# Optimization experiments

Measured on AMD Instinct MI355X. Metric: run time of the kernel, lower is better.

Reference implementation:

```python
import jax, jax.numpy as jnp
import numpy as np

D, H1, H2, OUT = 1024, 4096, 4096, 1


def _tanh_jet(a0, a1, a2):
    # 2nd-order Taylor-mode push-through of tanh:
    # u0 = tanh(a0); u1 = sech^2(a0)*a1; u2 = sech^2(a0)*a2 - 2*tanh(a0)*sech^2(a0)*a1^2
    u0 = jnp.tanh(a0)
    s = 1.0 - u0 * u0
    u1 = s * a1
    u2 = s * a2 - 2.0 * u0 * s * (a1 * a1)
    return u0, u1, u2


def setup_inputs() -> dict:
    key = jax.random.key(0)
    ks = jax.random.split(key, 7)
    x = jax.random.normal(ks[0], (D,), dtype=jnp.float32)
    # Kaiming-like scaling so tanh stays in its nonlinear regime
    W1 = jax.random.normal(ks[1], (H1, D), dtype=jnp.float32) / np.sqrt(D)
    b1 = jax.random.normal(ks[2], (H1,), dtype=jnp.float32) * 0.01
    W2 = jax.random.normal(ks[3], (H2, H1), dtype=jnp.float32) / np.sqrt(H1)
    b2 = jax.random.normal(ks[4], (H2,), dtype=jnp.float32) * 0.01
    W3 = jax.random.normal(ks[5], (OUT, H2), dtype=jnp.float32) / np.sqrt(H2)
    b3 = jax.random.normal(ks[6], (OUT,), dtype=jnp.float32) * 0.01
    return {"x": x, "W1": W1, "b1": b1, "W2": W2, "b2": b2, "W3": W3, "b3": b3}


def reference(x, W1, b1, W2, b2, W3, b3):
    # propagated simultaneously over all D basis tangent vectors (vectorized vmap).
    d = x.shape[0]
    X1 = jnp.eye(d, dtype=x.dtype)            # [D, D] basis tangents; x2 = 0
    # layer 1 (linear): primal broadcasts over the tangent batch
    a0 = x @ W1.T + b1                         # [H1]
    a1 = X1 @ W1.T                             # [D, H1]
    a2 = jnp.zeros_like(a1)                    # second input coefficient is zero
    u0, u1, u2 = _tanh_jet(a0, a1, a2)
    # layer 2 (linear)
    z0 = u0 @ W2.T + b2                        # [H2]
    z1 = u1 @ W2.T                             # [D, H2]
    z2 = u2 @ W2.T                             # [D, H2]
    v0, v1, v2 = _tanh_jet(z0, z1, z2)
    # layer 3 (linear); F2[i] = e_i^T H_f(x) e_i
    F2 = v2 @ W3.T                             # [D, 1]
    return F2.sum(0)                           # [1] = trace(H_f) = Laplacian
```

## Files before the change

### kernel.cpp

```cpp
#include <hip/hip_runtime.h>
#include <math.h>

#define DD 1024
#define HH1 4096
#define HH2 4096

typedef __attribute__((ext_vector_type(8))) short bf16x8;
typedef __attribute__((ext_vector_type(4))) float f32x4;
typedef unsigned short ushort_t;

#define WS_FAST_BYTES 42008576ull
#define K4_LDS_BYTES (131072 + 64)

__device__ inline void wave_reduce2(float& a, float& b) {
  #pragma unroll
  for (int off = 32; off > 0; off >>= 1) {
    a += __shfl_down(a, off, 64);
    b += __shfl_down(b, off, 64);
  }
}

__device__ inline unsigned int f2b(float f) {
  union { float f; unsigned int u; } v; v.f = f;
  return (v.u + 0x7FFFu + ((v.u >> 16) & 1u)) >> 16;
}
__device__ inline unsigned int pack2(float a, float b) {
  return f2b(a) | (f2b(b) << 16);
}

__device__ inline void gl_lds16(const void* g, void* l) {
  __builtin_amdgcn_global_load_lds(
      (const __attribute__((address_space(1))) unsigned int*)g,
      (__attribute__((address_space(3))) unsigned int*)l, 16, 0, 0);
}

__global__ __launch_bounds__(256) void kA2a_l1(
    const float* __restrict__ W1, const float* __restrict__ x,
    const float* __restrict__ b1, float* __restrict__ u0,
    float* __restrict__ q) {
  const int h = blockIdx.x;
  const int tid = threadIdx.x;
  const float4 w = ((const float4*)(W1 + (size_t)h * DD))[tid];
  const float4 xv = ((const float4*)x)[tid];
  float dot = w.x * xv.x + w.y * xv.y + w.z * xv.z + w.w * xv.w;
  float sq  = w.x * w.x + w.y * w.y + w.z * w.z + w.w * w.w;
  wave_reduce2(dot, sq);
  __shared__ float lds[8];
  const int lane = tid & 63, wid = tid >> 6;
  if (lane == 0) { lds[wid * 2] = dot; lds[wid * 2 + 1] = sq; }
  __syncthreads();
  if (tid == 0) {
    float dsum = lds[0] + lds[2] + lds[4] + lds[6];
    float rsum = lds[1] + lds[3] + lds[5] + lds[7];
    float a0 = dsum + b1[h];
    float u = tanhf(a0);
    float s = 1.f - u * u;
    u0[h] = u;
    q[h] = -2.f * u * s * rsum;
  }
}

#define TP 516
__global__ __launch_bounds__(256) void kA2b_t(
    const float* __restrict__ W1, ushort_t* __restrict__ Bp) {
  __shared__ ushort_t T[32 * TP];
  const int tid = threadIdx.x;
  const int h0 = (blockIdx.x >> 1) * 32;
  const int i0 = (blockIdx.x & 1) * 512;
  #pragma unroll
  for (int it = 0; it < 16; ++it) {
    const int lin = it * 256 + tid;
    const int r = lin >> 7;
    const int c4 = lin & 127;
    float4 w = *(const float4*)(W1 + (size_t)(h0 + r) * DD + i0 + c4 * 4);
    uint2 pk;
    pk.x = pack2(w.x, w.y);
    pk.y = pack2(w.z, w.w);
    *(uint2*)&T[r * TP + c4 * 4] = pk;
  }
  __syncthreads();
  const int ip = tid * 2;
  #pragma unroll
  for (int c = 0; c < 4; ++c) {
    unsigned int R[8];
    #pragma unroll
    for (int r8 = 0; r8 < 8; ++r8)
      R[r8] = *(const unsigned int*)&T[(c * 8 + r8) * TP + ip];
    unsigned int oa[4], ob[4];
    #pragma unroll
    for (int k2 = 0; k2 < 4; ++k2) {
      oa[k2] = (R[2 * k2] & 0xffffu) | (R[2 * k2 + 1] << 16);
      ob[k2] = (R[2 * k2] >> 16) | (R[2 * k2 + 1] & 0xffff0000u);
    }
    *(uint4*)(Bp + (size_t)(i0 + ip) * HH1 + h0 + c * 8) = *(const uint4*)oa;
    *(uint4*)(Bp + (size_t)(i0 + ip + 1) * HH1 + h0 + c * 8) = *(const uint4*)ob;
  }
}

__global__ __launch_bounds__(256) void k0a_layer2conv(
    const float* __restrict__ W2, const float* __restrict__ b2,
    const float* __restrict__ W3, const float* __restrict__ u0,
    const float* __restrict__ q, ushort_t* __restrict__ Ap,
    float* __restrict__ cv, float* __restrict__ cd) {
  int g = blockIdx.x;
  int tid = threadIdx.x;
  const float4* row = (const float4*)(W2 + (size_t)g * HH1);
  const float4* u4 = (const float4*)u0;
  const float4* q4 = (const float4*)q;
  float zacc = 0.f, dacc = 0.f;
  #pragma unroll
  for (int it = 0; it < 4; ++it) {
    int j = tid + it * 256;
    float4 w = row[j];
    float4 u = u4[j];
    float4 qq = q4[j];
    float4 sv;
    sv.x = 1.f - u.x * u.x;
    sv.y = 1.f - u.y * u.y;
    sv.z = 1.f - u.z * u.z;
    sv.w = 1.f - u.w * u.w;
    zacc += w.x * u.x + w.y * u.y + w.z * u.z + w.w * u.w;
    dacc += w.x * qq.x + w.y * qq.y + w.z * qq.z + w.w * qq.w;
    uint2 pk;
    pk.x = pack2(w.x * sv.x, w.y * sv.y);
    pk.y = pack2(w.z * sv.z, w.w * sv.w);
    *(uint2*)(Ap + (size_t)g * HH1 + j * 4) = pk;
  }
  wave_reduce2(zacc, dacc);
  __shared__ float lds[8];
  int lane = tid & 63, wid = tid >> 6;
  if (lane == 0) { lds[wid * 2] = zacc; lds[wid * 2 + 1] = dacc; }
  __syncthreads();
  if (tid == 0) {
    float z = lds[0] + lds[2] + lds[4] + lds[6] + b2[g];
    float d = lds[1] + lds[3] + lds[5] + lds[7];
    float v = tanhf(z);
    float t = 1.f - v * v;
    float c = W3[g] * t;
    cv[g] = c * v;
    cd[g] = c * d;
  }
}

__global__ __launch_bounds__(512) void k4_bt64q(
    const ushort_t* __restrict__ Ap, const ushort_t* __restrict__ Bp,
    const float* __restrict__ cv, float* __restrict__ P) {
  extern __shared__ __align__(16) char smem[];
  char* const Ab0 = smem;
  char* const Bb0 = smem + 65536;
  float* const red = (float*)(smem + 131072);

  const int tid = threadIdx.x;
  const int lane = tid & 63;
  const int wave = tid >> 6;
  const int wm = wave >> 1;
  const int wn = wave & 1;
  const int l = blockIdx.x;
  const int xcd = l & 7;
  const int jj = l >> 3;
  const int g0 = (xcd * 4 + (jj & 3)) * 128;
  const int i0 = (jj >> 2) * 128;

  const int srow = lane >> 3;
  const int schunk = (lane & 7) ^ srow;
  const size_t agbase = (size_t)(g0 + srow) * HH1 + schunk * 8;
  const size_t bgbase = (size_t)(i0 + srow) * HH1 + schunk * 8;

  const int fr = lane & 15;
  const int fc = lane >> 4;
  const int rsw = fr & 7;

  f32x4 acc[2][4];
  const f32x4 zero = {0.f, 0.f, 0.f, 0.f};
  #pragma unroll
  for (int mt = 0; mt < 2; ++mt)
    #pragma unroll
    for (int nt = 0; nt < 4; ++nt) acc[mt][nt] = zero;

  #define STAGE_PAIR(tile, sub) do {                                        \
      const int buf_ = (tile) & 3;                                          \
      const int r0_ = wave * 16 + (sub) * 8;                                \
      const size_t koff_ = (size_t)(((tile) & 63) * 64);                    \
      gl_lds16(Ap + agbase + (size_t)r0_ * HH1 + koff_,                     \
               Ab0 + buf_ * 16384 + r0_ * 128);                             \
      gl_lds16(Bp + bgbase + (size_t)r0_ * HH1 + koff_,                     \
               Bb0 + buf_ * 16384 + r0_ * 128);                             \
    } while (0)

  STAGE_PAIR(0, 0); STAGE_PAIR(0, 1);
  STAGE_PAIR(1, 0); STAGE_PAIR(1, 1);
  STAGE_PAIR(2, 0); STAGE_PAIR(2, 1);

  for (int t = 0; t < 64; ++t) {
    const int buf = t & 3;
    const char* Abuf = Ab0 + buf * 16384;
    const char* Bbuf = Bb0 + buf * 16384;
    asm volatile("s_waitcnt vmcnt(8)" ::: "memory");
    __builtin_amdgcn_s_barrier();
    asm volatile("" ::: "memory");
    #pragma unroll
    for (int kk = 0; kk < 2; ++kk) {
      STAGE_PAIR(t + 3, kk);
      bf16x8 af[2], bfv[4];
      #pragma unroll
      for (int mt = 0; mt < 2; ++mt) {
        const int row = wm * 32 + mt * 16 + fr;
        af[mt] = *(const bf16x8*)(Abuf + row * 128 + (((kk * 4 + fc) ^ rsw) * 16));
      }
      #pragma unroll
      for (int nt = 0; nt < 4; ++nt) {
        const int row = wn * 64 + nt * 16 + fr;
        bfv[nt] = *(const bf16x8*)(Bbuf + row * 128 + (((kk * 4 + fc) ^ rsw) * 16));
      }
      __builtin_amdgcn_s_setprio(1);
      #pragma unroll
      for (int mt = 0; mt < 2; ++mt)
        #pragma unroll
        for (int nt = 0; nt < 4; ++nt)
          acc[mt][nt] = __builtin_amdgcn_mfma_f32_16x16x32_bf16(
              af[mt], bfv[nt], acc[mt][nt], 0, 0, 0);
      __builtin_amdgcn_s_setprio(0);
      if (kk == 0) __builtin_amdgcn_s_barrier();
    }
  }
  #undef STAGE_PAIR

  float part = 0.f;
  #pragma unroll
  for (int mt = 0; mt < 2; ++mt) {
    #pragma unroll
    for (int r = 0; r < 4; ++r) {
      const int g = g0 + wm * 32 + mt * 16 + fc * 4 + r;
      const float c = cv[g];
      float ss = 0.f;
      #pragma unroll
      for (int nt = 0; nt < 4; ++nt) {
        float v = acc[mt][nt][r];
        ss += v * v;
      }
      part += c * ss;
    }
  }
  #pragma unroll
  for (int off = 32; off > 0; off >>= 1) part += __shfl_down(part, off, 64);
  if (lane == 0) red[wave] = part;
  __syncthreads();
  if (tid == 0) {
    float s = 0.f;
    #pragma unroll
    for (int w2 = 0; w2 < 8; ++w2) s += red[w2];
    P[l] = s;
  }
}

__global__ __launch_bounds__(256) void k5_final(
    const float* __restrict__ cd, const float* __restrict__ P,
    float* __restrict__ out) {
  int tid = threadIdx.x;
  float a = 0.f;
  for (int j = tid; j < HH2; j += 256) a += cd[j];
  float b = P[tid];
  float v = a - 2.f * b;
  #pragma unroll
  for (int off = 32; off > 0; off >>= 1) v += __shfl_down(v, off, 64);
  __shared__ float lds[4];
  int lane = tid & 63, wid = tid >> 6;
  if (lane == 0) lds[wid] = v;
  __syncthreads();
  if (tid == 0) out[0] = lds[0] + lds[1] + lds[2] + lds[3];
}


__global__ __launch_bounds__(256) void k1_slow(
    const float* __restrict__ W1, const float* __restrict__ x,
    const float* __restrict__ b1, float* __restrict__ u0,
    float* __restrict__ q, float* __restrict__ s_out,
    float* __restrict__ out) {
  int h = blockIdx.x;
  int tid = threadIdx.x;
  const float4* row = (const float4*)(W1 + (size_t)h * DD);
  const float4* x4 = (const float4*)x;
  float4 w = row[tid];
  float4 xv = x4[tid];
  float dot = w.x * xv.x + w.y * xv.y + w.z * xv.z + w.w * xv.w;
  float sq = w.x * w.x + w.y * w.y + w.z * w.z + w.w * w.w;
  wave_reduce2(dot, sq);
  __shared__ float lds[8];
  int lane = tid & 63, wid = tid >> 6;
  if (lane == 0) { lds[wid * 2] = dot; lds[wid * 2 + 1] = sq; }
  __syncthreads();
  if (tid == 0) {
    float dsum = lds[0] + lds[2] + lds[4] + lds[6];
    float rsum = lds[1] + lds[3] + lds[5] + lds[7];
    float a0 = dsum + b1[h];
    float u = tanhf(a0);
    float s = 1.f - u * u;
    u0[h] = u;
    s_out[h] = s;
    q[h] = -2.f * u * s * rsum;
    if (h == 0) out[0] = 0.f;
  }
}

__global__ __launch_bounds__(256) void k2_slow(
    const float* __restrict__ W2, const float* __restrict__ b2,
    const float* __restrict__ W3, const float* __restrict__ u0,
    const float* __restrict__ q, float* __restrict__ cv,
    float* __restrict__ out) {
  int g = blockIdx.x;
  int tid = threadIdx.x;
  const float4* row = (const float4*)(W2 + (size_t)g * HH1);
  const float4* u4 = (const float4*)u0;
  const float4* q4 = (const float4*)q;
  float zacc = 0.f, dacc = 0.f;
  for (int j = tid; j < HH1 / 4; j += 256) {
    float4 w = row[j];
    float4 u = u4[j];
    float4 qq = q4[j];
    zacc += w.x * u.x + w.y * u.y + w.z * u.z + w.w * u.w;
    dacc += w.x * qq.x + w.y * qq.y + w.z * qq.z + w.w * qq.w;
  }
  wave_reduce2(zacc, dacc);
  __shared__ float lds[8];
  int lane = tid & 63, wid = tid >> 6;
  if (lane == 0) { lds[wid * 2] = zacc; lds[wid * 2 + 1] = dacc; }
  __syncthreads();
  if (tid == 0) {
    float z = lds[0] + lds[2] + lds[4] + lds[6] + b2[g];
    float d = lds[1] + lds[3] + lds[5] + lds[7];
    float v = tanhf(z);
    float t = 1.f - v * v;
    float c = W3[g] * t;
    cv[g] = c * v;
    atomicAdd(out, c * d);
  }
}

__global__ __launch_bounds__(256) void k4_slow(
    const float* __restrict__ W2, const float* __restrict__ W1,
    const float* __restrict__ s, const float* __restrict__ cv,
    float* __restrict__ out) {
  __shared__ float As[32][68];
  __shared__ float Bs[32][68];
  int tid = threadIdx.x;
  int g0 = blockIdx.y * 64;
  int i0 = blockIdx.x * 64;
  int tr = (tid / 16) * 4;
  int tc = (tid % 16) * 4;
  float acc[4][4] = {};
  for (int k0 = 0; k0 < HH1; k0 += 32) {
    for (int ll = tid; ll < (64 * 32 / 4); ll += 256) {
      int row = ll / 8;
      int c4 = ll % 8;
      float4 w = *(const float4*)(W2 + (size_t)(g0 + row) * HH1 + k0 + c4 * 4);
      float4 sv = *(const float4*)(s + k0 + c4 * 4);
      As[c4 * 4 + 0][row] = w.x * sv.x;
      As[c4 * 4 + 1][row] = w.y * sv.y;
      As[c4 * 4 + 2][row] = w.z * sv.z;
      As[c4 * 4 + 3][row] = w.w * sv.w;
    }
    for (int ll = tid; ll < (32 * 64 / 4); ll += 256) {
      int row = ll / 16;
      int c4 = ll % 16;
      float4 w = *(const float4*)(W1 + (size_t)(k0 + row) * DD + i0 + c4 * 4);
      *(float4*)&Bs[row][c4 * 4] = w;
    }
    __syncthreads();
    #pragma unroll
    for (int k = 0; k < 32; ++k) {
      float4 av = *(const float4*)&As[k][tr];
      float4 bv = *(const float4*)&Bs[k][tc];
      float a_[4] = {av.x, av.y, av.z, av.w};
      float b_[4] = {bv.x, bv.y, bv.z, bv.w};
      #pragma unroll
      for (int r = 0; r < 4; ++r)
        #pragma unroll
        for (int c = 0; c < 4; ++c)
          acc[r][c] += a_[r] * b_[c];
    }
    __syncthreads();
  }
  float contrib = 0.f;
  #pragma unroll
  for (int r = 0; r < 4; ++r) {
    float ss = acc[r][0] * acc[r][0] + acc[r][1] * acc[r][1] +
               acc[r][2] * acc[r][2] + acc[r][3] * acc[r][3];
    contrib += cv[g0 + tr + r] * ss;
  }
  #pragma unroll
  for (int off = 32; off > 0; off >>= 1) contrib += __shfl_down(contrib, off, 64);
  __shared__ float red[4];
  int lane = tid & 63, wid = tid >> 6;
  if (lane == 0) red[wid] = contrib;
  __syncthreads();
  if (tid == 0) atomicAdd(out, -2.f * (red[0] + red[1] + red[2] + red[3]));
}

extern "C" void kernel_launch(void* const* d_in, const int* in_sizes, int n_in,
                              void* d_out, int out_size, void* d_ws, size_t ws_size,
                              hipStream_t stream) {
  const float* x  = (const float*)d_in[0];
  const float* W1 = (const float*)d_in[1];
  const float* b1 = (const float*)d_in[2];
  const float* W2 = (const float*)d_in[3];
  const float* b2 = (const float*)d_in[4];
  const float* W3 = (const float*)d_in[5];
  float* out = (float*)d_out;
  float* ws = (float*)d_ws;

  if (ws_size >= WS_FAST_BYTES) {
    float* u0 = ws;
    float* q  = ws + 4096;
    float* cv = ws + 8192;
    float* cd = ws + 12288;
    float* P  = ws;
    ushort_t* Ap = (ushort_t*)((char*)d_ws + 65536);
    ushort_t* Bp = (ushort_t*)((char*)d_ws + 33619968);
    hipFuncSetAttribute((const void*)k4_bt64q,
                        hipFuncAttributeMaxDynamicSharedMemorySize,
                        K4_LDS_BYTES);
    hipLaunchKernelGGL(kA2a_l1, dim3(HH1), dim3(256), 0, stream,
                       W1, x, b1, u0, q);
    hipLaunchKernelGGL(kA2b_t, dim3(256), dim3(256), 0, stream, W1, Bp);
    hipLaunchKernelGGL(k0a_layer2conv, dim3(HH2), dim3(256), 0, stream,
                       W2, b2, W3, u0, q, Ap, cv, cd);
    hipLaunchKernelGGL(k4_bt64q, dim3(256), dim3(512), K4_LDS_BYTES, stream,
                       Ap, Bp, cv, P);
    hipLaunchKernelGGL(k5_final, dim3(1), dim3(256), 0, stream, cd, P, out);
  } else {
    float* u0 = ws;
    float* q  = ws + 4096;
    float* s  = ws + 8192;
    float* cv = ws + 12288;
    hipLaunchKernelGGL(k1_slow, dim3(HH1), dim3(256), 0, stream,
                       W1, x, b1, u0, q, s, out);
    hipLaunchKernelGGL(k2_slow, dim3(HH2), dim3(256), 0, stream,
                       W2, b2, W3, u0, q, cv, out);
    hipLaunchKernelGGL(k4_slow, dim3(DD / 64, HH2 / 64), dim3(256), 0, stream,
                       W2, W1, s, cv, out);
  }
}
```

Baseline: 177.1 us.

## Use 32x32 MFMA with split-K wave groups and atomic final reduction

Rewrites the main GEMM kernel to use 32x32x16 bf16 MFMA tiles. The 8 waves are split into two groups that each handle alternate K tiles, with the two partial accumulators combined through LDS at the end. The final reduction kernel is dropped: the per-g correction term and the per-block partial sums are now added directly to the output with atomics, and the output is zeroed in the first kernel. This cuts LDS fragment loads per MFMA and removes one launch, at the cost of an extra LDS exchange and a float atomic ordering that is not deterministic.

```diff
diff --git a/kernel.cpp b/kernel.cpp
--- a/kernel.cpp
+++ b/kernel.cpp
@@ -7,10 +7,11 @@
 
 typedef __attribute__((ext_vector_type(8))) short bf16x8;
 typedef __attribute__((ext_vector_type(4))) float f32x4;
+typedef __attribute__((ext_vector_type(16))) float f32x16;
 typedef unsigned short ushort_t;
 
 #define WS_FAST_BYTES 42008576ull
-#define K4_LDS_BYTES (131072 + 64)
+#define K4_LDS_BYTES 131072
 
 __device__ inline void wave_reduce2(float& a, float& b) {
   #pragma unroll
@@ -37,9 +38,10 @@
 __global__ __launch_bounds__(256) void kA2a_l1(
     const float* __restrict__ W1, const float* __restrict__ x,
     const float* __restrict__ b1, float* __restrict__ u0,
-    float* __restrict__ q) {
+    float* __restrict__ q, float* __restrict__ out) {
   const int h = blockIdx.x;
   const int tid = threadIdx.x;
+  if (h == 0 && tid == 0) out[0] = 0.f;
   const float4 w = ((const float4*)(W1 + (size_t)h * DD))[tid];
   const float4 xv = ((const float4*)x)[tid];
   float dot = w.x * xv.x + w.y * xv.y + w.z * xv.z + w.w * xv.w;
@@ -101,7 +103,7 @@
     const float* __restrict__ W2, const float* __restrict__ b2,
     const float* __restrict__ W3, const float* __restrict__ u0,
     const float* __restrict__ q, ushort_t* __restrict__ Ap,
-    float* __restrict__ cv, float* __restrict__ cd) {
+    float* __restrict__ cv, float* __restrict__ out) {
   int g = blockIdx.x;
   int tid = threadIdx.x;
   const float4* row = (const float4*)(W2 + (size_t)g * HH1);
@@ -138,23 +140,21 @@
     float t = 1.f - v * v;
     float c = W3[g] * t;
     cv[g] = c * v;
-    cd[g] = c * d;
-  }
-}
-
-__global__ __launch_bounds__(512) void k4_bt64q(
+    atomicAdd(out, c * d);
+  }
+}
+
+__global__ __launch_bounds__(512) void k4_v3(
     const ushort_t* __restrict__ Ap, const ushort_t* __restrict__ Bp,
-    const float* __restrict__ cv, float* __restrict__ P) {
+    const float* __restrict__ cv, float* __restrict__ out) {
   extern __shared__ __align__(16) char smem[];
-  char* const Ab0 = smem;
-  char* const Bb0 = smem + 65536;
-  float* const red = (float*)(smem + 131072);
 
   const int tid = threadIdx.x;
   const int lane = tid & 63;
   const int wave = tid >> 6;
-  const int wm = wave >> 1;
-  const int wn = wave & 1;
+  const int gp = wave >> 2;
+  const int wq = wave & 3;
+  const int wm = wq >> 1, wn = wq & 1;
   const int l = blockIdx.x;
   const int xcd = l & 7;
   const int jj = l >> 3;
@@ -162,112 +162,112 @@
   const int i0 = (jj >> 2) * 128;
 
   const int srow = lane >> 3;
-  const int schunk = (lane & 7) ^ srow;
-  const size_t agbase = (size_t)(g0 + srow) * HH1 + schunk * 8;
-  const size_t bgbase = (size_t)(i0 + srow) * HH1 + schunk * 8;
-
-  const int fr = lane & 15;
-  const int fc = lane >> 4;
-  const int rsw = fr & 7;
-
-  f32x4 acc[2][4];
-  const f32x4 zero = {0.f, 0.f, 0.f, 0.f};
+  const int lchunk = (lane & 7) ^ srow;
+  const ushort_t* gA0 = Ap + (size_t)(g0 + wave * 16 + 0 + srow) * HH1 + lchunk * 8;
+  const ushort_t* gA1 = Ap + (size_t)(g0 + wave * 16 + 8 + srow) * HH1 + lchunk * 8;
+  const ushort_t* gB0 = Bp + (size_t)(i0 + wave * 16 + 0 + srow) * HH1 + lchunk * 8;
+  const ushort_t* gB1 = Bp + (size_t)(i0 + wave * 16 + 8 + srow) * HH1 + lchunk * 8;
+
+  const int half = lane >> 5;
+  const int r7 = lane & 7;
+  const int rowA0 = (wm * 64 + (lane & 31)) * 128;
+  const int rowA1 = rowA0 + 32 * 128;
+  const int rowB0 = 16384 + (wn * 64 + (lane & 31)) * 128;
+  const int rowB1 = rowB0 + 32 * 128;
+
+  f32x16 acc[2][2];
   #pragma unroll
   for (int mt = 0; mt < 2; ++mt)
     #pragma unroll
-    for (int nt = 0; nt < 4; ++nt) acc[mt][nt] = zero;
-
-  #define STAGE_PAIR(tile, sub) do {                                        \
-      const int buf_ = (tile) & 3;                                          \
-      const int r0_ = wave * 16 + (sub) * 8;                                \
-      const size_t koff_ = (size_t)(((tile) & 63) * 64);                    \
-      gl_lds16(Ap + agbase + (size_t)r0_ * HH1 + koff_,                     \
-               Ab0 + buf_ * 16384 + r0_ * 128);                             \
-      gl_lds16(Bp + bgbase + (size_t)r0_ * HH1 + koff_,                     \
-               Bb0 + buf_ * 16384 + r0_ * 128);                             \
+    for (int nt = 0; nt < 2; ++nt)
+      #pragma unroll
+      for (int r = 0; r < 16; ++r) acc[mt][nt][r] = 0.f;
+
+  #define STAGE(tile) do {                                              \
+      char* tb_ = smem + ((tile) & 3) * 32768;                          \
+      const int ko_ = ((tile) & 63) * 64;                               \
+      gl_lds16(gA0 + ko_, tb_ + (wave * 16 + 0) * 128 + lane * 16);     \
+      gl_lds16(gA1 + ko_, tb_ + (wave * 16 + 8) * 128 + lane * 16);     \
+      gl_lds16(gB0 + ko_, tb_ + 16384 + (wave * 16 + 0) * 128 + lane * 16); \
+      gl_lds16(gB1 + ko_, tb_ + 16384 + (wave * 16 + 8) * 128 + lane * 16); \
     } while (0)
 
-  STAGE_PAIR(0, 0); STAGE_PAIR(0, 1);
-  STAGE_PAIR(1, 0); STAGE_PAIR(1, 1);
-  STAGE_PAIR(2, 0); STAGE_PAIR(2, 1);
-
-  for (int t = 0; t < 64; ++t) {
-    const int buf = t & 3;
-    const char* Abuf = Ab0 + buf * 16384;
-    const char* Bbuf = Bb0 + buf * 16384;
+  STAGE(0); STAGE(1);
+  for (int s = 0; s < 32; ++s) {
+    STAGE(2 * s + 2);
+    STAGE(2 * s + 3);
     asm volatile("s_waitcnt vmcnt(8)" ::: "memory");
     __builtin_amdgcn_s_barrier();
     asm volatile("" ::: "memory");
-    #pragma unroll
-    for (int kk = 0; kk < 2; ++kk) {
-      STAGE_PAIR(t + 3, kk);
-      bf16x8 af[2], bfv[4];
+    const char* tb = smem + ((2 * s + gp) & 3) * 32768;
+    #pragma unroll
+    for (int kk = 0; kk < 4; ++kk) {
+      const int cb = ((kk * 2 + half) ^ r7) * 16;
+      bf16x8 af[2], bfv[2];
+      af[0]  = *(const bf16x8*)(tb + rowA0 + cb);
+      af[1]  = *(const bf16x8*)(tb + rowA1 + cb);
+      bfv[0] = *(const bf16x8*)(tb + rowB0 + cb);
+      bfv[1] = *(const bf16x8*)(tb + rowB1 + cb);
+      __builtin_amdgcn_s_setprio(1);
+      acc[0][0] = __builtin_amdgcn_mfma_f32_32x32x16_bf16(af[0], bfv[0], acc[0][0], 0, 0, 0);
+      acc[0][1] = __builtin_amdgcn_mfma_f32_32x32x16_bf16(af[0], bfv[1], acc[0][1], 0, 0, 0);
+      acc[1][0] = __builtin_amdgcn_mfma_f32_32x32x16_bf16(af[1], bfv[0], acc[1][0], 0, 0, 0);
+      acc[1][1] = __builtin_amdgcn_mfma_f32_32x32x16_bf16(af[1], bfv[1], acc[1][1], 0, 0, 0);
+      __builtin_amdgcn_s_setprio(0);
+    }
+    asm volatile("" ::: "memory");
+    __builtin_amdgcn_s_barrier();
+  }
+  #undef STAGE
+
+  asm volatile("s_waitcnt vmcnt(0)" ::: "memory");
+  __builtin_amdgcn_s_barrier();
+
+  char* xz = smem + 65536 + wq * 16384;
+  if (gp == 1) {
+    #pragma unroll
+    for (int qd = 0; qd < 16; ++qd) {
+      const int mt = qd >> 3, nt = (qd >> 2) & 1, r0 = (qd & 3) * 4;
+      float4 v;
+      v.x = acc[mt][nt][r0 + 0];
+      v.y = acc[mt][nt][r0 + 1];
+      v.z = acc[mt][nt][r0 + 2];
+      v.w = acc[mt][nt][r0 + 3];
+      *(float4*)(xz + qd * 1024 + ((lane + qd) & 63) * 16) = v;
+    }
+  }
+  __syncthreads();
+  if (gp == 0) {
+    #pragma unroll
+    for (int qd = 0; qd < 16; ++qd) {
+      const int mt = qd >> 3, nt = (qd >> 2) & 1, r0 = (qd & 3) * 4;
+      float4 v = *(const float4*)(xz + qd * 1024 + ((lane + qd) & 63) * 16);
+      acc[mt][nt][r0 + 0] += v.x;
+      acc[mt][nt][r0 + 1] += v.y;
+      acc[mt][nt][r0 + 2] += v.z;
+      acc[mt][nt][r0 + 3] += v.w;
+    }
+    float part = 0.f;
+    #pragma unroll
+    for (int mt = 0; mt < 2; ++mt) {
       #pragma unroll
-      for (int mt = 0; mt < 2; ++mt) {
-        const int row = wm * 32 + mt * 16 + fr;
-        af[mt] = *(const bf16x8*)(Abuf + row * 128 + (((kk * 4 + fc) ^ rsw) * 16));
+      for (int r = 0; r < 16; ++r) {
+        const int g = g0 + wm * 64 + mt * 32 + (r & 3) + 8 * (r >> 2) + 4 * half;
+        const float c = cv[g];
+        const float m0 = acc[mt][0][r];
+        const float m1 = acc[mt][1][r];
+        part += c * (m0 * m0 + m1 * m1);
       }
-      #pragma unroll
-      for (int nt = 0; nt < 4; ++nt) {
-        const int row = wn * 64 + nt * 16 + fr;
-        bfv[nt] = *(const bf16x8*)(Bbuf + row * 128 + (((kk * 4 + fc) ^ rsw) * 16));
-      }
-      __builtin_amdgcn_s_setprio(1);
-      #pragma unroll
-      for (int mt = 0; mt < 2; ++mt)
-        #pragma unroll
-        for (int nt = 0; nt < 4; ++nt)
-          acc[mt][nt] = __builtin_amdgcn_mfma_f32_16x16x32_bf16(
-              af[mt], bfv[nt], acc[mt][nt], 0, 0, 0);
-      __builtin_amdgcn_s_setprio(0);
-      if (kk == 0) __builtin_amdgcn_s_barrier();
-    }
-  }
-  #undef STAGE_PAIR
-
-  float part = 0.f;
-  #pragma unroll
-  for (int mt = 0; mt < 2; ++mt) {
-    #pragma unroll
-    for (int r = 0; r < 4; ++r) {
-      const int g = g0 + wm * 32 + mt * 16 + fc * 4 + r;
-      const float c = cv[g];
-      float ss = 0.f;
-      #pragma unroll
-      for (int nt = 0; nt < 4; ++nt) {
-        float v = acc[mt][nt][r];
-        ss += v * v;
-      }
-      part += c * ss;
-    }
-  }
-  #pragma unroll
-  for (int off = 32; off > 0; off >>= 1) part += __shfl_down(part, off, 64);
-  if (lane == 0) red[wave] = part;
+    }
+    #pragma unroll
+    for (int off = 32; off > 0; off >>= 1) part += __shfl_down(part, off, 64);
+    if (lane == 0) ((float*)smem)[wq] = part;
+  }
   __syncthreads();
   if (tid == 0) {
-    float s = 0.f;
-    #pragma unroll
-    for (int w2 = 0; w2 < 8; ++w2) s += red[w2];
-    P[l] = s;
-  }
-}
-
-__global__ __launch_bounds__(256) void k5_final(
-    const float* __restrict__ cd, const float* __restrict__ P,
-    float* __restrict__ out) {
-  int tid = threadIdx.x;
-  float a = 0.f;
-  for (int j = tid; j < HH2; j += 256) a += cd[j];
-  float b = P[tid];
-  float v = a - 2.f * b;
-  #pragma unroll
-  for (int off = 32; off > 0; off >>= 1) v += __shfl_down(v, off, 64);
-  __shared__ float lds[4];
-  int lane = tid & 63, wid = tid >> 6;
-  if (lane == 0) lds[wid] = v;
-  __syncthreads();
-  if (tid == 0) out[0] = lds[0] + lds[1] + lds[2] + lds[3];
+    float* rp = (float*)smem;
+    atomicAdd(out, -2.f * (rp[0] + rp[1] + rp[2] + rp[3]));
+  }
 }
 
 
@@ -412,21 +412,18 @@
     float* u0 = ws;
     float* q  = ws + 4096;
     float* cv = ws + 8192;
-    float* cd = ws + 12288;
-    float* P  = ws;
     ushort_t* Ap = (ushort_t*)((char*)d_ws + 65536);
     ushort_t* Bp = (ushort_t*)((char*)d_ws + 33619968);
-    hipFuncSetAttribute((const void*)k4_bt64q,
+    hipFuncSetAttribute((const void*)k4_v3,
                         hipFuncAttributeMaxDynamicSharedMemorySize,
                         K4_LDS_BYTES);
     hipLaunchKernelGGL(kA2a_l1, dim3(HH1), dim3(256), 0, stream,
-                       W1, x, b1, u0, q);
+                       W1, x, b1, u0, q, out);
     hipLaunchKernelGGL(kA2b_t, dim3(256), dim3(256), 0, stream, W1, Bp);
     hipLaunchKernelGGL(k0a_layer2conv, dim3(HH2), dim3(256), 0, stream,
-                       W2, b2, W3, u0, q, Ap, cv, cd);
-    hipLaunchKernelGGL(k4_bt64q, dim3(256), dim3(512), K4_LDS_BYTES, stream,
-                       Ap, Bp, cv, P);
-    hipLaunchKernelGGL(k5_final, dim3(1), dim3(256), 0, stream, cd, P, out);
+                       W2, b2, W3, u0, q, Ap, cv, out);
+    hipLaunchKernelGGL(k4_v3, dim3(256), dim3(512), K4_LDS_BYTES, stream,
+                       Ap, Bp, cv, out);
   } else {
     float* u0 = ws;
     float* q  = ws + 4096;
```

Result: slower. 208.8 us (+17.9%).

## Fuse layer-1 jet reduction with W1 bf16 transpose into one kernel

Applied to the files above, without the earlier changes.

Merges the layer-1 dot/sumsq kernel and the W1 bf16 transpose kernel into a single kernel, so W1 is read from global memory once instead of twice and one launch is removed. Each block now handles 16 rows over the full 1024 columns, with a 16-lane shuffle reduction. Separately, the layer-2 conversion kernel issues all of its W2/u0/q loads up front to raise memory-level parallelism. The trade-offs are fewer rows per block (256 blocks total) and more registers held in the layer-2 kernel.

```diff
diff --git a/kernel.cpp b/kernel.cpp
--- a/kernel.cpp
+++ b/kernel.cpp
@@ -34,66 +34,62 @@
       (__attribute__((address_space(3))) unsigned int*)l, 16, 0, 0);
 }
 
-__global__ __launch_bounds__(256) void kA2a_l1(
+#define TP2 1032
+__global__ __launch_bounds__(256) void kA3_l1t(
     const float* __restrict__ W1, const float* __restrict__ x,
     const float* __restrict__ b1, float* __restrict__ u0,
-    float* __restrict__ q) {
-  const int h = blockIdx.x;
+    float* __restrict__ q, ushort_t* __restrict__ Bp) {
+  __shared__ __align__(16) ushort_t T[16 * TP2];
   const int tid = threadIdx.x;
-  const float4 w = ((const float4*)(W1 + (size_t)h * DD))[tid];
-  const float4 xv = ((const float4*)x)[tid];
-  float dot = w.x * xv.x + w.y * xv.y + w.z * xv.z + w.w * xv.w;
-  float sq  = w.x * w.x + w.y * w.y + w.z * w.z + w.w * w.w;
-  wave_reduce2(dot, sq);
-  __shared__ float lds[8];
-  const int lane = tid & 63, wid = tid >> 6;
-  if (lane == 0) { lds[wid * 2] = dot; lds[wid * 2 + 1] = sq; }
-  __syncthreads();
-  if (tid == 0) {
-    float dsum = lds[0] + lds[2] + lds[4] + lds[6];
-    float rsum = lds[1] + lds[3] + lds[5] + lds[7];
-    float a0 = dsum + b1[h];
+  const int h0 = blockIdx.x * 16;
+  const int r = tid >> 4;
+  const int c = tid & 15;
+  const float4* rp = (const float4*)(W1 + (size_t)(h0 + r) * DD);
+  const float4* x4 = (const float4*)x;
+  float dot = 0.f, sq = 0.f;
+  #pragma unroll
+  for (int j = 0; j < 16; ++j) {
+    const int f = c + j * 16;
+    float4 wv = rp[f];
+    float4 xv = x4[f];
+    dot += wv.x * xv.x + wv.y * xv.y + wv.z * xv.z + wv.w * xv.w;
+    sq  += wv.x * wv.x + wv.y * wv.y + wv.z * wv.z + wv.w * wv.w;
+    uint2 pk;
+    pk.x = pack2(wv.x, wv.y);
+    pk.y = pack2(wv.z, wv.w);
+    *(uint2*)&T[r * TP2 + f * 4] = pk;
+  }
+  #pragma unroll
+  for (int off = 8; off > 0; off >>= 1) {
+    dot += __shfl_down(dot, off, 16);
+    sq  += __shfl_down(sq, off, 16);
+  }
+  if (c == 0) {
+    float a0 = dot + b1[h0 + r];
     float u = tanhf(a0);
     float s = 1.f - u * u;
-    u0[h] = u;
-    q[h] = -2.f * u * s * rsum;
-  }
-}
-
-#define TP 516
-__global__ __launch_bounds__(256) void kA2b_t(
-    const float* __restrict__ W1, ushort_t* __restrict__ Bp) {
-  __shared__ ushort_t T[32 * TP];
-  const int tid = threadIdx.x;
-  const int h0 = (blockIdx.x >> 1) * 32;
-  const int i0 = (blockIdx.x & 1) * 512;
-  #pragma unroll
-  for (int it = 0; it < 16; ++it) {
-    const int lin = it * 256 + tid;
-    const int r = lin >> 7;
-    const int c4 = lin & 127;
-    float4 w = *(const float4*)(W1 + (size_t)(h0 + r) * DD + i0 + c4 * 4);
-    uint2 pk;
-    pk.x = pack2(w.x, w.y);
-    pk.y = pack2(w.z, w.w);
-    *(uint2*)&T[r * TP + c4 * 4] = pk;
-  }
-  __syncthreads();
-  const int ip = tid * 2;
-  #pragma unroll
-  for (int c = 0; c < 4; ++c) {
-    unsigned int R[8];
-    #pragma unroll
-    for (int r8 = 0; r8 < 8; ++r8)
-      R[r8] = *(const unsigned int*)&T[(c * 8 + r8) * TP + ip];
-    unsigned int oa[4], ob[4];
-    #pragma unroll
-    for (int k2 = 0; k2 < 4; ++k2) {
-      oa[k2] = (R[2 * k2] & 0xffffu) | (R[2 * k2 + 1] << 16);
-      ob[k2] = (R[2 * k2] >> 16) | (R[2 * k2 + 1] & 0xffff0000u);
-    }
-    *(uint4*)(Bp + (size_t)(i0 + ip) * HH1 + h0 + c * 8) = *(const uint4*)oa;
-    *(uint4*)(Bp + (size_t)(i0 + ip + 1) * HH1 + h0 + c * 8) = *(const uint4*)ob;
+    u0[h0 + r] = u;
+    q[h0 + r] = -2.f * u * s * sq;
+  }
+  __syncthreads();
+  #pragma unroll
+  for (int rep = 0; rep < 2; ++rep) {
+    const int ip = rep * 512 + tid * 2;
+    #pragma unroll
+    for (int cg = 0; cg < 2; ++cg) {
+      unsigned int R[8];
+      #pragma unroll
+      for (int r8 = 0; r8 < 8; ++r8)
+        R[r8] = *(const unsigned int*)&T[(cg * 8 + r8) * TP2 + ip];
+      unsigned int oa[4], ob[4];
+      #pragma unroll
+      for (int k2 = 0; k2 < 4; ++k2) {
+        oa[k2] = (R[2 * k2] & 0xffffu) | (R[2 * k2 + 1] << 16);
+        ob[k2] = (R[2 * k2] >> 16) | (R[2 * k2 + 1] & 0xffff0000u);
+      }
+      *(uint4*)(Bp + (size_t)ip * HH1 + h0 + cg * 8) = *(const uint4*)oa;
+      *(uint4*)(Bp + (size_t)(ip + 1) * HH1 + h0 + cg * 8) = *(const uint4*)ob;
+    }
   }
 }
 
@@ -107,23 +103,29 @@
   const float4* row = (const float4*)(W2 + (size_t)g * HH1);
   const float4* u4 = (const float4*)u0;
   const float4* q4 = (const float4*)q;
+  float4 w[4], u[4], qq[4];
+  #pragma unroll
+  for (int it = 0; it < 4; ++it) w[it] = row[tid + it * 256];
+  #pragma unroll
+  for (int it = 0; it < 4; ++it) u[it] = u4[tid + it * 256];
+  #pragma unroll
+  for (int it = 0; it < 4; ++it) qq[it] = q4[tid + it * 256];
   float zacc = 0.f, dacc = 0.f;
   #pragma unroll
   for (int it = 0; it < 4; ++it) {
-    int j = tid + it * 256;
-    float4 w = row[j];
-    float4 u = u4[j];
-    float4 qq = q4[j];
+    const int j = tid + it * 256;
     float4 sv;
-    sv.x = 1.f - u.x * u.x;
-    sv.y = 1.f - u.y * u.y;
-    sv.z = 1.f - u.z * u.z;
-    sv.w = 1.f - u.w * u.w;
-    zacc += w.x * u.x + w.y * u.y + w.z * u.z + w.w * u.w;
-    dacc += w.x * qq.x + w.y * qq.y + w.z * qq.z + w.w * qq.w;
+    sv.x = 1.f - u[it].x * u[it].x;
+    sv.y = 1.f - u[it].y * u[it].y;
+    sv.z = 1.f - u[it].z * u[it].z;
+    sv.w = 1.f - u[it].w * u[it].w;
+    zacc += w[it].x * u[it].x + w[it].y * u[it].y +
+            w[it].z * u[it].z + w[it].w * u[it].w;
+    dacc += w[it].x * qq[it].x + w[it].y * qq[it].y +
+            w[it].z * qq[it].z + w[it].w * qq[it].w;
     uint2 pk;
-    pk.x = pack2(w.x * sv.x, w.y * sv.y);
-    pk.y = pack2(w.z * sv.z, w.w * sv.w);
+    pk.x = pack2(w[it].x * sv.x, w[it].y * sv.y);
+    pk.y = pack2(w[it].z * sv.z, w[it].w * sv.w);
     *(uint2*)(Ap + (size_t)g * HH1 + j * 4) = pk;
   }
   wave_reduce2(zacc, dacc);
@@ -419,9 +421,8 @@
     hipFuncSetAttribute((const void*)k4_bt64q,
                         hipFuncAttributeMaxDynamicSharedMemorySize,
                         K4_LDS_BYTES);
-    hipLaunchKernelGGL(kA2a_l1, dim3(HH1), dim3(256), 0, stream,
-                       W1, x, b1, u0, q);
-    hipLaunchKernelGGL(kA2b_t, dim3(256), dim3(256), 0, stream, W1, Bp);
+    hipLaunchKernelGGL(kA3_l1t, dim3(256), dim3(256), 0, stream,
+                       W1, x, b1, u0, q, Bp);
     hipLaunchKernelGGL(k0a_layer2conv, dim3(HH2), dim3(256), 0, stream,
                        W2, b2, W3, u0, q, Ap, cv, cd);
     hipLaunchKernelGGL(k4_bt64q, dim3(256), dim3(512), K4_LDS_BYTES, stream,
```

Measured after the change: 171.2 us. 1.03x faster.
